# Kernel optimization log

Hardware: AMD Instinct MI355X
Metric: run time of the kernel (lower is better)

## Reference

```python
import jax, jax.numpy as jnp
import numpy as np

B = 16384
STATE = 524   # state_dim / output_size
IENC = 256    # INet output dim
ZD = 32       # z_dim
H = 256       # expert hidden size
E = 5         # num_experts
HG = 256      # gating hidden size
IN1 = STATE + IENC + ZD   # 812, PredictionNet layer-1 input
IN2 = H + ZD              # 288, layers 2/3 input


def _uni(k, shape):
    # matches PredictionNet.init_params glorot-style uniform bound
    bound = float(np.sqrt(6.0 / (shape[-2] * shape[-1])))
    return jax.random.uniform(k, shape, jnp.float32, -bound, bound)


def setup_inputs() -> dict:
    key = jax.random.key(0)
    ks = jax.random.split(key, 12)
    d = {}
    d['z'] = jax.random.normal(ks[0], (B, ZD), jnp.float32)
    d['p_prev'] = jax.random.normal(ks[1], (B, STATE), jnp.float32)
    d['I'] = jax.random.normal(ks[2], (B, 2048), jnp.float32)
    # gating network: (state+z) -> HG -> HG//2 -> E
    d['gw1'] = _uni(ks[3], (STATE + ZD, HG)); d['gb1'] = jnp.zeros((HG,), jnp.float32)
    d['gw2'] = _uni(ks[4], (HG, HG // 2));    d['gb2'] = jnp.zeros((HG // 2,), jnp.float32)
    d['gw3'] = _uni(ks[5], (HG // 2, E));     d['gb3'] = jnp.zeros((E,), jnp.float32)
    # INet: 2048 -> 256 -> 256 -> 256
    d['iw1'] = _uni(ks[6], (2048, IENC)); d['ib1'] = jnp.zeros((IENC,), jnp.float32)
    d['iw2'] = _uni(ks[7], (IENC, IENC)); d['ib2'] = jnp.zeros((IENC,), jnp.float32)
    d['iw3'] = _uni(ks[8], (IENC, IENC)); d['ib3'] = jnp.zeros((IENC,), jnp.float32)
    # expert weights [E, in, out], biases [E, out]
    d['w_l1'] = _uni(ks[9], (E, IN1, H));     d['b_l1'] = jnp.zeros((E, H), jnp.float32)
    d['w_l2'] = _uni(ks[10], (E, IN2, H));    d['b_l2'] = jnp.zeros((E, H), jnp.float32)
    d['w_l3'] = _uni(ks[11], (E, IN2, STATE)); d['b_l3'] = jnp.zeros((E, STATE), jnp.float32)
    return d


def reference(z, p_prev, I, gw1, gb1, gw2, gb2, gw3, gb3,
              iw1, ib1, iw2, ib2, iw3, ib3,
              w_l1, b_l1, w_l2, b_l2, w_l3, b_l3):
    elu = jax.nn.elu
    # gating network -> softmax blending coefficients omega [B, E]
    g = elu(jnp.concatenate([z, p_prev], axis=1) @ gw1 + gb1)
    g = elu(g @ gw2 + gb2)
    omega = jax.nn.softmax(g @ gw3 + gb3, axis=-1)
    # interaction encoder
    Ienc = elu(elu(elu(I @ iw1 + ib1) @ iw2 + ib2) @ iw3 + ib3)
    x = jnp.concatenate([p_prev, Ienc], axis=1)  # [B, STATE+IENC]

    def moe_linear(h, W, b):
        # same math as sum_e omega_e * (h @ W_e) + omega @ b, without
        # materializing per-sample blended [B, in, out] weights
        per_expert = jnp.einsum('bi,eio->beo', h, W)
        return jnp.einsum('be,beo->bo', omega, per_expert) + omega @ b

    h0 = jnp.concatenate([z, x], axis=1)          # [B, 812]
    h1 = elu(moe_linear(h0, w_l1, b_l1))          # [B, 256]
    h2 = elu(moe_linear(jnp.concatenate([z, h1], axis=1), w_l2, b_l2))
    h3 = moe_linear(jnp.concatenate([z, h2], axis=1), w_l3, b_l3)  # [B, 524]
    return h3
```

## Files before the change

### kernel.cpp

```cpp
#include <hip/hip_runtime.h>
#include <hip/hip_bf16.h>
#include <cstdint>
#include <cstddef>


#define BATCH 16384

typedef __attribute__((ext_vector_type(8))) short short8;
typedef __attribute__((ext_vector_type(4))) float f32x4;
typedef unsigned short u16;
typedef unsigned int u32;

typedef __attribute__((address_space(3))) void lds_t;
typedef __attribute__((address_space(1))) void gmem_t;

__device__ __forceinline__ void gload16(const u16* g, u16* l) {
  __builtin_amdgcn_global_load_lds((gmem_t*)(u16*)g, (lds_t*)l, 16, 0, 0);
}

__device__ __forceinline__ float bf2f(u16 u) {
  union { float f; u32 i; } v; v.i = ((u32)u) << 16; return v.f;
}
__device__ __forceinline__ u16 f2bf(float f) {
  union { float f; u32 i; } v; v.f = f;
  u32 x = v.i;
  return (u16)((x + 0x7fffu + ((x >> 16) & 1u)) >> 16);
}
__device__ __forceinline__ u16 load_bf(const void* p, long i, int f32) {
  return f32 ? f2bf(((const float*)p)[i]) : ((const u16*)p)[i];
}
__device__ __forceinline__ float elu_f(float x) { return x > 0.f ? x : expm1f(x); }

__device__ __forceinline__ int swz(int row, int q) { return q ^ ((row >> 1) & 3); }

__global__ __launch_bounds__(256) void detect_dtype(const u32* __restrict__ zr,
                                                    int* __restrict__ flag)
{
  __shared__ int cnt;
  if (threadIdx.x == 0) cnt = 0;
  __syncthreads();
  u32 w = zr[threadIdx.x];
  int e = (w >> 7) & 0xFF;
  if (e >= 112 && e <= 142) atomicAdd(&cnt, 1);
  __syncthreads();
  if (threadIdx.x == 0) *flag = (cnt < 128) ? 1 : 0;
}

__global__ __launch_bounds__(256) void prep_kernel(
    const void* __restrict__ z, const void* __restrict__ p,
    const int* __restrict__ flagp,
    u16* __restrict__ h0, u16* __restrict__ h1c, u16* __restrict__ h2c,
    const void* ib1, const void* ib2, const void* ib3,
    const void* gb1, const void* gb2, const void* gb3,
    const void* gw3, const void* bl1, const void* bl2, const void* bl3,
    u16* __restrict__ smallc)
{
  const int f32 = *flagp;
  const int b = blockIdx.y;
  const int c = blockIdx.x * 256 + threadIdx.x;
  if (blockIdx.y == 0 && blockIdx.x == 0) {
    for (long j = threadIdx.x; j < 7100; j += 256) {
      u16 v;
      if      (j < 256)  v = load_bf(ib1, j,        f32);
      else if (j < 512)  v = load_bf(ib2, j - 256,  f32);
      else if (j < 768)  v = load_bf(ib3, j - 512,  f32);
      else if (j < 1024) v = load_bf(gb1, j - 768,  f32);
      else if (j < 1152) v = load_bf(gb2, j - 1024, f32);
      else if (j < 1280) v = (j - 1152 < 5) ? load_bf(gb3, j - 1152, f32) : (u16)0;
      else if (j < 1920) v = load_bf(gw3, j - 1280, f32);
      else if (j < 3200) v = load_bf(bl1, j - 1920, f32);
      else if (j < 4480) v = load_bf(bl2, j - 3200, f32);
      else               v = load_bf(bl3, j - 4480, f32);
      smallc[j] = v;
    }
  }
  if (c >= 832) return;
  const long i = (long)b * 832 + c;
  if (c < 32) {
    u16 v = load_bf(z, (long)b * 32 + c, f32);
    h0[i] = v;
    h1c[(long)b * 288 + c] = v;
    h2c[(long)b * 288 + c] = v;
  } else if (c < 556) {
    h0[i] = load_bf(p, (long)b * 524 + (c - 32), f32);
  } else if (c >= 812) {
    h0[i] = 0;
  }
}

__global__ __launch_bounds__(256) void convert_I(
    const void* __restrict__ I, const int* __restrict__ flagp,
    u16* __restrict__ out)
{
  const int f32 = *flagp;
  const long total8 = (long)BATCH * 2048 / 8;
  const long stride = (long)gridDim.x * blockDim.x;
  for (long t = (long)blockIdx.x * blockDim.x + threadIdx.x; t < total8; t += stride) {
    if (f32) {
      const float4* src = (const float4*)I;
      float4 a = src[t * 2], b = src[t * 2 + 1];
      union { u16 r[8]; uint4 v; } u;
      u.r[0] = f2bf(a.x); u.r[1] = f2bf(a.y); u.r[2] = f2bf(a.z); u.r[3] = f2bf(a.w);
      u.r[4] = f2bf(b.x); u.r[5] = f2bf(b.y); u.r[6] = f2bf(b.z); u.r[7] = f2bf(b.w);
      *(uint4*)(out + t * 8) = u.v;
    } else {
      *(uint4*)(out + t * 8) = ((const uint4*)I)[t];
    }
  }
}

struct TPSeg { long end; int K, N, Kp, Np; };

__global__ __launch_bounds__(256) void transpose_all(
    const int* __restrict__ flagp,
    const void* s0, const void* s1, const void* s2, const void* s3,
    const void* s4, const void* s5, const void* s6, const void* s7,
    u16* d0, u16* d1, u16* d2, u16* d3, u16* d4, u16* d5, u16* d6, u16* d7)
{
  const TPSeg seg[8] = {
    {  524288, 2048, 256, 2048, 256 },
    {  589824,  256, 256,  256, 256 },
    {  655360,  256, 256,  256, 256 },
    {  802816,  556, 256,  576, 256 },
    {  835584,  256, 128,  256, 128 },
    { 1900544,  812, 256,  832, 256 },
    { 2269184,  288, 256,  288, 256 },
    { 3098624,  288, 524,  288, 576 },
  };
  const void* const srcs[8] = { s0, s1, s2, s3, s4, s5, s6, s7 };
  u16* const dsts[8] = { d0, d1, d2, d3, d4, d5, d6, d7 };
  const int f32 = *flagp;
  const long total = 3098624;
  const long stride = (long)gridDim.x * blockDim.x;
  for (long i = (long)blockIdx.x * blockDim.x + threadIdx.x; i < total; i += stride) {
    int s = 0;
    long base = 0;
    while (i >= seg[s].end) { base = seg[s].end; ++s; }
    const long j = i - base;
    const int Kp = seg[s].Kp, Np = seg[s].Np, K = seg[s].K, N = seg[s].N;
    const int k = (int)(j % Kp);
    const long t = j / Kp;
    const int n = (int)(t % Np);
    const int e = (int)(t / Np);
    u16 v = 0;
    if (k < K && n < N) v = load_bf(srcs[s], (long)e * K * N + (long)k * N + n, f32);
    dsts[s][j] = v;
  }
}

template<bool ELU>
__global__ __launch_bounds__(256) void gemm128(
    const u16* __restrict__ A, int lda,
    const u16* __restrict__ Wt, int ldw,
    const u16* __restrict__ bias,
    u16* __restrict__ C, int ldc, int col_off, int K)
{
  __shared__ __align__(16) u16 sA[128 * 32];
  __shared__ __align__(16) u16 sB[128 * 32];

  const int tid  = threadIdx.x;
  const int bm   = blockIdx.x, bn = blockIdx.y;
  const int lane = tid & 63, wave = tid >> 6;
  const int wm = (wave & 1) * 64, wn = (wave >> 1) * 64;
  const int lrow = lane & 15, lq = lane >> 4;

  const int srow0 = 32 * wave + (lane >> 2);
  const int sq    = (lane & 3) ^ ((lane >> 3) & 3);
  const u16* Ag = A  + (size_t)(bm * 128 + srow0) * lda + sq * 8;
  const u16* Wg = Wt + (size_t)(bn * 128 + srow0) * ldw + sq * 8;
  u16* lA = sA + wave * 1024;
  u16* lB = sB + wave * 1024;

  f32x4 acc[4][4] = {};

  for (int k0 = 0; k0 < K; k0 += 32) {
    __syncthreads();
    gload16(Ag + k0, lA);
    gload16(Ag + (size_t)16 * lda + k0, lA + 512);
    gload16(Wg + k0, lB);
    gload16(Wg + (size_t)16 * ldw + k0, lB + 512);
    __syncthreads();

    short8 a[4], b[4];
#pragma unroll
    for (int i = 0; i < 4; ++i) {
      const int r = wm + i * 16 + lrow;
      a[i] = *(const short8*)(sA + r * 32 + swz(r, lq) * 8);
    }
#pragma unroll
    for (int i = 0; i < 4; ++i) {
      const int r = wn + i * 16 + lrow;
      b[i] = *(const short8*)(sB + r * 32 + swz(r, lq) * 8);
    }

#pragma unroll
    for (int mi = 0; mi < 4; ++mi)
#pragma unroll
      for (int ni = 0; ni < 4; ++ni)
        acc[mi][ni] = __builtin_amdgcn_mfma_f32_16x16x32_bf16(a[mi], b[ni], acc[mi][ni], 0, 0, 0);
  }

#pragma unroll
  for (int ni = 0; ni < 4; ++ni) {
    const int col = bn * 128 + wn + ni * 16 + lrow;
    const float bv = bf2f(bias[col]);
#pragma unroll
    for (int mi = 0; mi < 4; ++mi) {
#pragma unroll
      for (int r = 0; r < 4; ++r) {
        const int row = bm * 128 + wm + mi * 16 + lq * 4 + r;
        float v = acc[mi][ni][r] + bv;
        if (ELU) v = elu_f(v);
        C[(size_t)row * ldc + col_off + col] = f2bf(v);
      }
    }
  }
}

__global__ __launch_bounds__(256) void gating3_kernel(
    const u16* __restrict__ g2, const u16* __restrict__ gw3c,
    const u16* __restrict__ gb3c, float* __restrict__ omega)
{
  const int wid  = (blockIdx.x << 2) + (threadIdx.x >> 6);
  const int lane = threadIdx.x & 63;
  const u32 gp = *(const u32*)(g2 + (size_t)wid * 128 + lane * 2);
  const float x0 = bf2f((u16)(gp & 0xffffu));
  const float x1 = bf2f((u16)(gp >> 16));
  float acc[5];
#pragma unroll
  for (int e = 0; e < 5; ++e)
    acc[e] = x0 * bf2f(gw3c[(lane * 2) * 5 + e]) + x1 * bf2f(gw3c[(lane * 2 + 1) * 5 + e]);
#pragma unroll
  for (int off = 1; off < 64; off <<= 1) {
#pragma unroll
    for (int e = 0; e < 5; ++e) acc[e] += __shfl_xor(acc[e], off);
  }
  if (lane == 0) {
    float t[5], m = -1e30f;
#pragma unroll
    for (int e = 0; e < 5; ++e) { t[e] = acc[e] + bf2f(gb3c[e]); m = fmaxf(m, t[e]); }
    float s = 0.f;
#pragma unroll
    for (int e = 0; e < 5; ++e) { t[e] = expf(t[e] - m); s += t[e]; }
    const float inv = 1.f / s;
#pragma unroll
    for (int e = 0; e < 5; ++e) omega[(size_t)wid * 5 + e] = t[e] * inv;
  }
}

template<bool ELU>
__global__ __launch_bounds__(256, 2) void moe_gemm(
    const u16* __restrict__ A, int lda,
    const u16* __restrict__ Wt, int ldw, long wstride_e,
    const u16* __restrict__ bias, int bias_n,
    const float* __restrict__ omega,
    void* __restrict__ C, int ldc, int col_off, int n_store, int K,
    const int* __restrict__ flagp, int is_final)
{
  __shared__ __align__(16) u16 sA[128 * 32];
  __shared__ __align__(16) u16 sW[5][64 * 32];
  __shared__ float som[128 * 5];
  __shared__ float sbias[5][64];

  const int tid  = threadIdx.x;
  const int bm   = blockIdx.x, bn = blockIdx.y;
  const int lane = tid & 63, wave = tid >> 6;
  const int wm = (wave & 1) * 64, wn = (wave >> 1) * 32;
  const int lrow = lane & 15, lq = lane >> 4;
  const int f32out = is_final ? *flagp : 0;

  for (int t = tid; t < 960; t += 256) {
    if (t < 640) {
      som[t] = omega[(size_t)(bm * 128) * 5 + t];
    } else {
      const int j = t - 640;
      const int e = j >> 6, c = j & 63;
      const int col = bn * 64 + c;
      sbias[e][c] = (col < bias_n) ? bf2f(bias[(size_t)e * bias_n + col]) : 0.f;
    }
  }

  const int sq = (lane & 3) ^ ((lane >> 3) & 3);
  const int srowA = 32 * wave + (lane >> 2);
  const int srowW = 16 * wave + (lane >> 2);
  const u16* Ag = A  + (size_t)(bm * 128 + srowA) * lda + sq * 8;
  const u16* Wg = Wt + (size_t)(bn * 64 + srowW) * ldw + sq * 8;
  u16* lA = sA + wave * 1024;
  const int lWoff = wave * 512;

  f32x4 acc[5][4][2] = {};

  for (int k0 = 0; k0 < K; k0 += 32) {
    __syncthreads();
    gload16(Ag + k0, lA);
    gload16(Ag + (size_t)16 * lda + k0, lA + 512);
#pragma unroll
    for (int e = 0; e < 5; ++e)
      gload16(Wg + e * wstride_e + k0, sW[e] + lWoff);
    __syncthreads();

    short8 a[4];
#pragma unroll
    for (int i = 0; i < 4; ++i) {
      const int r = wm + i * 16 + lrow;
      a[i] = *(const short8*)(sA + r * 32 + swz(r, lq) * 8);
    }
    const int rb0 = wn + lrow, rb1 = rb0 + 16;
    const int ob0 = rb0 * 32 + swz(rb0, lq) * 8;
    const int ob1 = rb1 * 32 + swz(rb1, lq) * 8;
#pragma unroll
    for (int e = 0; e < 5; ++e) {
      short8 b0 = *(const short8*)(sW[e] + ob0);
      short8 b1 = *(const short8*)(sW[e] + ob1);
#pragma unroll
      for (int mi = 0; mi < 4; ++mi) {
        acc[e][mi][0] = __builtin_amdgcn_mfma_f32_16x16x32_bf16(a[mi], b0, acc[e][mi][0], 0, 0, 0);
        acc[e][mi][1] = __builtin_amdgcn_mfma_f32_16x16x32_bf16(a[mi], b1, acc[e][mi][1], 0, 0, 0);
      }
    }
  }

#pragma unroll
  for (int mi = 0; mi < 4; ++mi) {
#pragma unroll
    for (int r = 0; r < 4; ++r) {
      const int rl = wm + mi * 16 + lq * 4 + r;
      const int row = bm * 128 + rl;
      float om[5];
#pragma unroll
      for (int e = 0; e < 5; ++e) om[e] = som[rl * 5 + e];
#pragma unroll
      for (int ni = 0; ni < 2; ++ni) {
        const int c = wn + ni * 16 + lrow;
        const int col = bn * 64 + c;
        if (col < n_store) {
          float v = 0.f;
#pragma unroll
          for (int e = 0; e < 5; ++e) v += om[e] * (acc[e][mi][ni][r] + sbias[e][c]);
          if (ELU) v = elu_f(v);
          const size_t idx = (size_t)row * ldc + col_off + col;
          if (f32out) ((float*)C)[idx] = v;
          else        ((u16*)C)[idx]   = f2bf(v);
        }
      }
    }
  }
}

extern "C" void kernel_launch(void* const* d_in, const int* in_sizes, int n_in,
                              void* d_out, int out_size, void* d_ws, size_t ws_size,
                              hipStream_t stream)
{
  const void* z    = d_in[0];
  const void* pprev= d_in[1];
  const void* I    = d_in[2];
  const void* gw1  = d_in[3];
  const void* gb1  = d_in[4];
  const void* gw2  = d_in[5];
  const void* gb2  = d_in[6];
  const void* gw3  = d_in[7];
  const void* gb3  = d_in[8];
  const void* iw1  = d_in[9];
  const void* ib1  = d_in[10];
  const void* iw2  = d_in[11];
  const void* ib2  = d_in[12];
  const void* iw3  = d_in[13];
  const void* ib3  = d_in[14];
  const void* wl1  = d_in[15];
  const void* bl1  = d_in[16];
  const void* wl2  = d_in[17];
  const void* bl2  = d_in[18];
  const void* wl3  = d_in[19];
  const void* bl3  = d_in[20];

  char* base = (char*)d_ws;
  size_t off = 0;
  auto alloc = [&](size_t bytes) -> void* {
    void* p = base + off;
    off = (off + bytes + 255) & ~(size_t)255;
    return p;
  };

  const size_t B = BATCH;
  int* flagp   = (int*)alloc(256);
  u16* h0      = (u16*)alloc(B * 832 * 2);
  u16* h1c     = (u16*)alloc(B * 288 * 2);
  u16* h2c     = (u16*)alloc(B * 288 * 2);
  u16* i1      = (u16*)alloc(B * 256 * 2);
  u16* i2      = (u16*)alloc(B * 256 * 2);
  float* omega = (float*)alloc(B * 5 * 4);
  u16* Ibf     = (u16*)alloc(B * 2048 * 2);
  u16* smallc  = (u16*)alloc(7100 * 2);
  u16* iw1t = (u16*)alloc((size_t)256 * 2048 * 2);
  u16* iw2t = (u16*)alloc((size_t)256 * 256 * 2);
  u16* iw3t = (u16*)alloc((size_t)256 * 256 * 2);
  u16* gw1t = (u16*)alloc((size_t)256 * 576 * 2);
  u16* gw2t = (u16*)alloc((size_t)128 * 256 * 2);
  u16* wl1t = (u16*)alloc((size_t)5 * 256 * 832 * 2);
  u16* wl2t = (u16*)alloc((size_t)5 * 256 * 288 * 2);
  u16* wl3t = (u16*)alloc((size_t)5 * 576 * 288 * 2);
  u16* g1 = i1;
  u16* g2 = i2;
  (void)in_sizes; (void)n_in; (void)out_size; (void)ws_size;

  u16* ib1c = smallc + 0,   *ib2c = smallc + 256, *ib3c = smallc + 512;
  u16* gb1c = smallc + 768, *gb2c = smallc + 1024, *gb3c = smallc + 1152;
  u16* gw3c = smallc + 1280;
  u16* bl1c = smallc + 1920, *bl2c = smallc + 3200, *bl3c = smallc + 4480;

  detect_dtype<<<1, 256, 0, stream>>>((const u32*)z, flagp);
  prep_kernel<<<dim3(4, BATCH), 256, 0, stream>>>(z, pprev, flagp, h0, h1c, h2c,
      ib1, ib2, ib3, gb1, gb2, gb3, gw3, bl1, bl2, bl3, smallc);
  convert_I<<<4096, 256, 0, stream>>>(I, flagp, Ibf);
  transpose_all<<<3072, 256, 0, stream>>>(flagp,
      iw1, iw2, iw3, gw1, gw2, wl1, wl2, wl3,
      iw1t, iw2t, iw3t, gw1t, gw2t, wl1t, wl2t, wl3t);

  gemm128<true><<<dim3(BATCH/128, 2), 256, 0, stream>>>(Ibf, 2048, iw1t, 2048, ib1c, i1, 256, 0,   2048);
  gemm128<true><<<dim3(BATCH/128, 2), 256, 0, stream>>>(i1,  256,  iw2t, 256,  ib2c, i2, 256, 0,   256);
  gemm128<true><<<dim3(BATCH/128, 2), 256, 0, stream>>>(i2,  256,  iw3t, 256,  ib3c, h0, 832, 556, 256);

  gemm128<true><<<dim3(BATCH/128, 2), 256, 0, stream>>>(h0, 832, gw1t, 576, gb1c, g1, 256, 0, 576);
  gemm128<true><<<dim3(BATCH/128, 1), 256, 0, stream>>>(g1, 256, gw2t, 256, gb2c, g2, 128, 0, 256);
  gating3_kernel<<<BATCH/4, 256, 0, stream>>>(g2, gw3c, gb3c, omega);

  moe_gemm<true><<<dim3(BATCH/128, 4), 256, 0, stream>>>(
      h0, 832, wl1t, 832, (long)256 * 832, bl1c, 256, omega, h1c, 288, 32, 256, 832, flagp, 0);
  moe_gemm<true><<<dim3(BATCH/128, 4), 256, 0, stream>>>(
      h1c, 288, wl2t, 288, (long)256 * 288, bl2c, 256, omega, h2c, 288, 32, 256, 288, flagp, 0);
  moe_gemm<false><<<dim3(BATCH/128, 9), 256, 0, stream>>>(
      h2c, 288, wl3t, 288, (long)576 * 288, bl3c, 524, omega, d_out, 524, 0, 524, 288, flagp, 1);
}
```

Baseline: 588.7 us.

## Double-buffer LDS tiles in dense and MoE GEMMs, shrink dense M tile to 64

Both the dense GEMM and the MoE GEMM now keep two LDS buffers and issue the global-to-LDS loads for the next K step before computing the current one. This leaves one barrier per iteration instead of two, so load latency can overlap with MFMA work. The dense GEMM also drops from 128-row to 64-row tiles with two blocks per CU, doubling its grid to improve occupancy on the many CUs. The cost is doubled LDS use in the MoE kernel, which may limit occupancy there, and less data reuse per block in the dense GEMM.

```diff
diff --git a/kernel.cpp b/kernel.cpp
--- a/kernel.cpp
+++ b/kernel.cpp
@@ -149,55 +149,65 @@
 }
 
 template<bool ELU>
-__global__ __launch_bounds__(256) void gemm128(
+__global__ __launch_bounds__(256, 2) void gemm64(
     const u16* __restrict__ A, int lda,
     const u16* __restrict__ Wt, int ldw,
     const u16* __restrict__ bias,
     u16* __restrict__ C, int ldc, int col_off, int K)
 {
-  __shared__ __align__(16) u16 sA[128 * 32];
-  __shared__ __align__(16) u16 sB[128 * 32];
+  __shared__ __align__(16) u16 sA[2][64 * 32];
+  __shared__ __align__(16) u16 sB[2][128 * 32];
 
   const int tid  = threadIdx.x;
   const int bm   = blockIdx.x, bn = blockIdx.y;
   const int lane = tid & 63, wave = tid >> 6;
-  const int wm = (wave & 1) * 64, wn = (wave >> 1) * 64;
+  const int wm = (wave & 1) * 32, wn = (wave >> 1) * 64;
   const int lrow = lane & 15, lq = lane >> 4;
 
-  const int srow0 = 32 * wave + (lane >> 2);
   const int sq    = (lane & 3) ^ ((lane >> 3) & 3);
-  const u16* Ag = A  + (size_t)(bm * 128 + srow0) * lda + sq * 8;
-  const u16* Wg = Wt + (size_t)(bn * 128 + srow0) * ldw + sq * 8;
-  u16* lA = sA + wave * 1024;
-  u16* lB = sB + wave * 1024;
-
-  f32x4 acc[4][4] = {};
-
-  for (int k0 = 0; k0 < K; k0 += 32) {
-    __syncthreads();
-    gload16(Ag + k0, lA);
-    gload16(Ag + (size_t)16 * lda + k0, lA + 512);
-    gload16(Wg + k0, lB);
-    gload16(Wg + (size_t)16 * ldw + k0, lB + 512);
-    __syncthreads();
-
-    short8 a[4], b[4];
-#pragma unroll
-    for (int i = 0; i < 4; ++i) {
+  const int srowA = 16 * wave + (lane >> 2);
+  const int srowB = 32 * wave + (lane >> 2);
+  const u16* Ag = A  + (size_t)(bm * 64  + srowA) * lda + sq * 8;
+  const u16* Wg = Wt + (size_t)(bn * 128 + srowB) * ldw + sq * 8;
+  const int laOff = wave * 512;
+  const int lbOff = wave * 1024;
+
+  f32x4 acc[2][4] = {};
+  const int nt = K / 32;
+
+  gload16(Ag, sA[0] + laOff);
+  gload16(Wg, sB[0] + lbOff);
+  gload16(Wg + (size_t)16 * ldw, sB[0] + lbOff + 512);
+  __syncthreads();
+
+  for (int t = 0; t < nt; ++t) {
+    const int cur = t & 1;
+    if (t + 1 < nt) {
+      const int k0 = (t + 1) * 32;
+      gload16(Ag + k0, sA[cur ^ 1] + laOff);
+      gload16(Wg + k0, sB[cur ^ 1] + lbOff);
+      gload16(Wg + (size_t)16 * ldw + k0, sB[cur ^ 1] + lbOff + 512);
+    }
+
+    short8 a[2], b[4];
+#pragma unroll
+    for (int i = 0; i < 2; ++i) {
       const int r = wm + i * 16 + lrow;
-      a[i] = *(const short8*)(sA + r * 32 + swz(r, lq) * 8);
+      a[i] = *(const short8*)(sA[cur] + r * 32 + swz(r, lq) * 8);
     }
 #pragma unroll
     for (int i = 0; i < 4; ++i) {
       const int r = wn + i * 16 + lrow;
-      b[i] = *(const short8*)(sB + r * 32 + swz(r, lq) * 8);
-    }
-
-#pragma unroll
-    for (int mi = 0; mi < 4; ++mi)
+      b[i] = *(const short8*)(sB[cur] + r * 32 + swz(r, lq) * 8);
+    }
+
+#pragma unroll
+    for (int mi = 0; mi < 2; ++mi)
 #pragma unroll
       for (int ni = 0; ni < 4; ++ni)
         acc[mi][ni] = __builtin_amdgcn_mfma_f32_16x16x32_bf16(a[mi], b[ni], acc[mi][ni], 0, 0, 0);
+
+    __syncthreads();
   }
 
 #pragma unroll
@@ -205,10 +215,10 @@
     const int col = bn * 128 + wn + ni * 16 + lrow;
     const float bv = bf2f(bias[col]);
 #pragma unroll
-    for (int mi = 0; mi < 4; ++mi) {
+    for (int mi = 0; mi < 2; ++mi) {
 #pragma unroll
       for (int r = 0; r < 4; ++r) {
-        const int row = bm * 128 + wm + mi * 16 + lq * 4 + r;
+        const int row = bm * 64 + wm + mi * 16 + lq * 4 + r;
         float v = acc[mi][ni][r] + bv;
         if (ELU) v = elu_f(v);
         C[(size_t)row * ldc + col_off + col] = f2bf(v);
@@ -257,8 +267,8 @@
     void* __restrict__ C, int ldc, int col_off, int n_store, int K,
     const int* __restrict__ flagp, int is_final)
 {
-  __shared__ __align__(16) u16 sA[128 * 32];
-  __shared__ __align__(16) u16 sW[5][64 * 32];
+  __shared__ __align__(16) u16 sA[2][128 * 32];
+  __shared__ __align__(16) u16 sW[2][5][64 * 32];
   __shared__ float som[128 * 5];
   __shared__ float sbias[5][64];
 
@@ -268,6 +278,23 @@
   const int wm = (wave & 1) * 64, wn = (wave >> 1) * 32;
   const int lrow = lane & 15, lq = lane >> 4;
   const int f32out = is_final ? *flagp : 0;
+
+  const int sq = (lane & 3) ^ ((lane >> 3) & 3);
+  const int srowA = 32 * wave + (lane >> 2);
+  const int srowW = 16 * wave + (lane >> 2);
+  const u16* Ag = A  + (size_t)(bm * 128 + srowA) * lda + sq * 8;
+  const u16* Wg = Wt + (size_t)(bn * 64 + srowW) * ldw + sq * 8;
+  const int laOff = wave * 1024;
+  const int lWoff = wave * 512;
+
+  f32x4 acc[5][4][2] = {};
+  const int nt = K / 32;
+
+  gload16(Ag, sA[0] + laOff);
+  gload16(Ag + (size_t)16 * lda, sA[0] + laOff + 512);
+#pragma unroll
+  for (int e = 0; e < 5; ++e)
+    gload16(Wg + e * wstride_e, sW[0][e] + lWoff);
 
   for (int t = tid; t < 960; t += 256) {
     if (t < 640) {
@@ -279,45 +306,40 @@
       sbias[e][c] = (col < bias_n) ? bf2f(bias[(size_t)e * bias_n + col]) : 0.f;
     }
   }
-
-  const int sq = (lane & 3) ^ ((lane >> 3) & 3);
-  const int srowA = 32 * wave + (lane >> 2);
-  const int srowW = 16 * wave + (lane >> 2);
-  const u16* Ag = A  + (size_t)(bm * 128 + srowA) * lda + sq * 8;
-  const u16* Wg = Wt + (size_t)(bn * 64 + srowW) * ldw + sq * 8;
-  u16* lA = sA + wave * 1024;
-  const int lWoff = wave * 512;
-
-  f32x4 acc[5][4][2] = {};
-
-  for (int k0 = 0; k0 < K; k0 += 32) {
-    __syncthreads();
-    gload16(Ag + k0, lA);
-    gload16(Ag + (size_t)16 * lda + k0, lA + 512);
-#pragma unroll
-    for (int e = 0; e < 5; ++e)
-      gload16(Wg + e * wstride_e + k0, sW[e] + lWoff);
-    __syncthreads();
+  __syncthreads();
+
+  for (int t = 0; t < nt; ++t) {
+    const int cur = t & 1;
+    if (t + 1 < nt) {
+      const int k0 = (t + 1) * 32;
+      gload16(Ag + k0, sA[cur ^ 1] + laOff);
+      gload16(Ag + (size_t)16 * lda + k0, sA[cur ^ 1] + laOff + 512);
+#pragma unroll
+      for (int e = 0; e < 5; ++e)
+        gload16(Wg + e * wstride_e + k0, sW[cur ^ 1][e] + lWoff);
+    }
 
     short8 a[4];
 #pragma unroll
     for (int i = 0; i < 4; ++i) {
       const int r = wm + i * 16 + lrow;
-      a[i] = *(const short8*)(sA + r * 32 + swz(r, lq) * 8);
+      a[i] = *(const short8*)(sA[cur] + r * 32 + swz(r, lq) * 8);
     }
     const int rb0 = wn + lrow, rb1 = rb0 + 16;
     const int ob0 = rb0 * 32 + swz(rb0, lq) * 8;
     const int ob1 = rb1 * 32 + swz(rb1, lq) * 8;
 #pragma unroll
     for (int e = 0; e < 5; ++e) {
-      short8 b0 = *(const short8*)(sW[e] + ob0);
-      short8 b1 = *(const short8*)(sW[e] + ob1);
+      short8 b0 = *(const short8*)(sW[cur][e] + ob0);
+      short8 b1 = *(const short8*)(sW[cur][e] + ob1);
 #pragma unroll
       for (int mi = 0; mi < 4; ++mi) {
         acc[e][mi][0] = __builtin_amdgcn_mfma_f32_16x16x32_bf16(a[mi], b0, acc[e][mi][0], 0, 0, 0);
         acc[e][mi][1] = __builtin_amdgcn_mfma_f32_16x16x32_bf16(a[mi], b1, acc[e][mi][1], 0, 0, 0);
       }
     }
+
+    __syncthreads();
   }
 
 #pragma unroll
@@ -416,12 +438,12 @@
       iw1, iw2, iw3, gw1, gw2, wl1, wl2, wl3,
       iw1t, iw2t, iw3t, gw1t, gw2t, wl1t, wl2t, wl3t);
 
-  gemm128<true><<<dim3(BATCH/128, 2), 256, 0, stream>>>(Ibf, 2048, iw1t, 2048, ib1c, i1, 256, 0,   2048);
-  gemm128<true><<<dim3(BATCH/128, 2), 256, 0, stream>>>(i1,  256,  iw2t, 256,  ib2c, i2, 256, 0,   256);
-  gemm128<true><<<dim3(BATCH/128, 2), 256, 0, stream>>>(i2,  256,  iw3t, 256,  ib3c, h0, 832, 556, 256);
-
-  gemm128<true><<<dim3(BATCH/128, 2), 256, 0, stream>>>(h0, 832, gw1t, 576, gb1c, g1, 256, 0, 576);
-  gemm128<true><<<dim3(BATCH/128, 1), 256, 0, stream>>>(g1, 256, gw2t, 256, gb2c, g2, 128, 0, 256);
+  gemm64<true><<<dim3(BATCH/64, 2), 256, 0, stream>>>(Ibf, 2048, iw1t, 2048, ib1c, i1, 256, 0,   2048);
+  gemm64<true><<<dim3(BATCH/64, 2), 256, 0, stream>>>(i1,  256,  iw2t, 256,  ib2c, i2, 256, 0,   256);
+  gemm64<true><<<dim3(BATCH/64, 2), 256, 0, stream>>>(i2,  256,  iw3t, 256,  ib3c, h0, 832, 556, 256);
+
+  gemm64<true><<<dim3(BATCH/64, 2), 256, 0, stream>>>(h0, 832, gw1t, 576, gb1c, g1, 256, 0, 576);
+  gemm64<true><<<dim3(BATCH/64, 1), 256, 0, stream>>>(g1, 256, gw2t, 256, gb2c, g2, 128, 0, 256);
   gating3_kernel<<<BATCH/4, 256, 0, stream>>>(g2, gw3c, gb3c, omega);
 
   moe_gemm<true><<<dim3(BATCH/128, 4), 256, 0, stream>>>(
```

New measurement: 557.9 us. -5.2%, faster.
